# Kernel optimization log

Hardware: AMD Instinct MI355X
Metric: run time of the kernel (lower is better)

Reference implementation:

```python
import jax, jax.numpy as jnp
import numpy as np

EMBED = 1024
ADIM = 1024
H = 16
HD = ADIM // H          # 64
RAY = 48                # ray_subdim
R = RAY // 3            # 16
SCALE = 1.0 / np.sqrt(HD)
NB = 768                # boundary tokens
MN = 8                  # max neighbors
FG = 6                  # face_group
L = 1024                # tokens per face
B = 12                  # b * face_group
STAGES = 4


def _apply_dray(x, d, einsum_str, inverse):
    ray = x[..., :RAY].reshape(x.shape[:-1] + (3, R))
    if inverse:
        d = jnp.swapaxes(d, -1, -2)
    ray = jnp.einsum(einsum_str, d, ray).reshape(x.shape[:-1] + (RAY,))
    return jnp.concatenate([ray, x[..., RAY:]], axis=-1)


def setup_inputs() -> dict:
    key = jax.random.key(0)
    ks = jax.random.split(key, 12)
    inp = {}
    inp['x'] = jax.random.normal(ks[0], (B, L, EMBED), dtype=jnp.float32)
    inp['qkv_w'] = jax.random.normal(ks[1], (EMBED, 3 * ADIM), dtype=jnp.float32) * 0.02
    inp['out_w'] = jax.random.normal(ks[2], (ADIM, EMBED), dtype=jnp.float32) * 0.02
    inp['out_b'] = jax.random.normal(ks[3], (EMBED,), dtype=jnp.float32) * 0.02
    inp['d_ray'] = jax.random.normal(ks[4], (STAGES, FG, L, 3, 3), dtype=jnp.float32)
    inp['boundary_face_ids'] = jax.random.randint(ks[5], (NB,), 0, FG, dtype=jnp.int32).astype(jnp.int64)
    inp['boundary_token_indices'] = jnp.arange(NB, dtype=jnp.int64)
    inp['boundary_local_indices'] = jax.random.randint(ks[6], (NB,), 0, L, dtype=jnp.int32).astype(jnp.int64)
    inp['boundary_stage_ids'] = jax.random.randint(ks[7], (NB,), 0, STAGES, dtype=jnp.int32).astype(jnp.int64)
    inp['neighbor_face_ids'] = jax.random.randint(ks[8], (NB, MN), 0, FG, dtype=jnp.int32).astype(jnp.int64)
    inp['neighbor_token_indices'] = jax.random.randint(ks[9], (NB, MN), 0, L, dtype=jnp.int32).astype(jnp.int64)
    inp['neighbor_local_indices'] = jax.random.randint(ks[10], (NB, MN), 0, L, dtype=jnp.int32).astype(jnp.int64)
    inp['neighbor_stage_ids'] = jax.random.randint(ks[11], (NB, MN), 0, STAGES, dtype=jnp.int32).astype(jnp.int64)
    inp['neighbor_mask'] = jnp.ones((NB, MN), dtype=bool)
    inp['face_group'] = FG
    return inp


def reference(x, qkv_w, out_w, out_b, d_ray,
              boundary_face_ids, boundary_token_indices, boundary_local_indices, boundary_stage_ids,
              neighbor_face_ids, neighbor_token_indices, neighbor_local_indices, neighbor_stage_ids,
              neighbor_mask, face_group):
    b = x.shape[0] // face_group
    l = x.shape[1]
    xt = x.reshape(b, face_group, l, EMBED)          # [b, FG, L, E]
    max_face, max_idx = face_group - 1, l - 1

    qf = jnp.clip(boundary_face_ids, 0, max_face)
    qi = jnp.clip(boundary_token_indices, 0, max_idx)
    valid_q = (boundary_face_ids == qf) & (boundary_token_indices == qi)

    nf = jnp.clip(neighbor_face_ids, 0, max_face)
    ni = jnp.clip(neighbor_token_indices, 0, max_idx)
    mask = neighbor_mask & (neighbor_face_ids == nf) & (neighbor_token_indices == ni)

    # gather boundary queries and neighbor keys/values
    x_q = xt[:, qf, qi, :]                            # [b, NB, E]
    x_kv = xt[:, nf, ni, :]                           # [b, NB, MN, E]
    q = (x_q @ qkv_w)[..., :ADIM]
    kv = x_kv @ qkv_w
    k = kv[..., ADIM:2 * ADIM]
    v = kv[..., 2 * ADIM:]

    nb, mn = q.shape[1], k.shape[2]
    q = q.reshape(b, nb, H, HD)
    k = k.reshape(b, nb, mn, H, HD)
    v = v.reshape(b, nb, mn, H, HD)

    d_q = d_ray[boundary_stage_ids, boundary_face_ids, boundary_local_indices]     # [NB, 3, 3]
    d_k = d_ray[neighbor_stage_ids,
                jnp.maximum(neighbor_face_ids, 0),
                jnp.maximum(neighbor_local_indices, 0)]                            # [NB, MN, 3, 3]

    q = _apply_dray(q, d_q, 'nij,bnhjr->bnhir', inverse=False)
    k = _apply_dray(k, d_k, 'nmij,bnmhjr->bnmhir', inverse=False)
    v = _apply_dray(v, d_k, 'nmij,bnmhjr->bnmhir', inverse=False)

    attn = jnp.einsum('bnhd,bnmhd->bnmh', q, k) * SCALE
    attn = jnp.where(mask[None, :, :, None], attn, -jnp.inf)
    attn = jax.nn.softmax(attn, axis=2)               # softmax over neighbors
    out = jnp.einsum('bnmh,bnmhd->bnhd', attn, v)

    out = _apply_dray(out, d_q, 'nij,bnhjr->bnhir', inverse=True)
    out = out.reshape(b, nb, ADIM) @ out_w + out_b
    out = out * valid_q[None, :, None].astype(out.dtype)

    out_full = jnp.zeros_like(xt).at[:, qf, qi, :].set(out)
    return out_full.reshape(-1, l, EMBED)
```

## Files before the change

kernel.cpp:

```cpp
#include <hip/hip_runtime.h>
#include <hip/hip_bf16.h>
#include <cstddef>

#define FG 6
#define L 1024
#define NB 768
#define MN 8
#define H 16
#define HD 64
#define ADIM 1024
#define STAGES 4
#define SCALE 0.125f

typedef __attribute__((ext_vector_type(8))) short bf16x8;
typedef __attribute__((ext_vector_type(4))) float f32x4;
typedef __attribute__((address_space(3))) short lds_short_t;
typedef const __attribute__((address_space(1))) short g_short_t;

__device__ __forceinline__ int clampi(int v, int lo, int hi) {
  return v < lo ? lo : (v > hi ? hi : v);
}

__device__ __forceinline__ short f2bf(float f) {
  __hip_bfloat16 h = __float2bfloat16(f);
  return *reinterpret_cast<short*>(&h);
}

__device__ __forceinline__ void gload16(const short* g, short* l) {
  __builtin_amdgcn_global_load_lds((g_short_t*)g, (lds_short_t*)l, 16, 0, 0);
}

__global__ __launch_bounds__(256)
void conv_bf16(const float* __restrict__ in, short* __restrict__ out) {
  size_t i = ((size_t)blockIdx.x * 256 + threadIdx.x) * 8;
  float4 a = *(const float4*)(in + i);
  float4 b = *(const float4*)(in + i + 4);
  bf16x8 v;
  v[0] = f2bf(a.x); v[1] = f2bf(a.y); v[2] = f2bf(a.z); v[3] = f2bf(a.w);
  v[4] = f2bf(b.x); v[5] = f2bf(b.y); v[6] = f2bf(b.z); v[7] = f2bf(b.w);
  *(bf16x8*)(out + i) = v;
}

__global__ __launch_bounds__(256)
void transpose_conv(const float* __restrict__ in, short* __restrict__ out,
                    int K, int N) {
  __shared__ float tile[32][33];
  const int n0 = blockIdx.x * 32, k0 = blockIdx.y * 32;
  const int tx = threadIdx.x & 31, ty = threadIdx.x >> 5;
  #pragma unroll
  for (int i = 0; i < 4; ++i)
    tile[ty + i * 8][tx] = in[(size_t)(k0 + ty + i * 8) * N + n0 + tx];
  __syncthreads();
  #pragma unroll
  for (int i = 0; i < 4; ++i)
    out[(size_t)(n0 + ty + i * 8) * K + k0 + tx] =
        f2bf(tile[tx][ty + i * 8]);
}

template<int MODE>
__global__ __launch_bounds__(256)
void mfma_gemm(const short* __restrict__ A, const short* __restrict__ B,
               void* __restrict__ Cv,
               const int* __restrict__ f_ids, const int* __restrict__ t_ids,
               const float* __restrict__ bias)
{
  constexpr int KT    = 16;
  constexpr int BCOL0 = (MODE == 1) ? 1024 : 0;

  __shared__ __align__(16) short As[8192];
  __shared__ __align__(16) short Bs[8192];

  const int tid  = threadIdx.x;
  const int w    = tid >> 6, lane = tid & 63;
  const int row0 = blockIdx.y * 128, col0 = blockIdx.x * 128;

  size_t aoff[4], boff[4];
  short *adst[4], *bdst[4];
  #pragma unroll
  for (int c = 0; c < 4; ++c) {
    const int d = (w * 4 + c) * 64 + lane;
    const int r = d >> 3;
    const int ssrc = (d & 7) ^ (r & 7);
    long gr;
    if (MODE == 2) {
      gr = row0 + r;
    } else {
      const int rr = row0 + r;
      int bi, idx;
      if (MODE == 0) { bi = rr >= NB;          idx = rr - bi * NB; }
      else           { bi = rr >= NB * MN;     idx = rr - bi * NB * MN; }
      const int f = clampi(f_ids[idx], 0, FG - 1);
      const int q = clampi(t_ids[idx], 0, L - 1);
      gr = (long)(bi * FG + f) * L + q;
    }
    aoff[c] = (size_t)gr * 1024 + ssrc * 8;
    boff[c] = (size_t)(BCOL0 + col0 + r) * 1024 + ssrc * 8;
    adst[c] = As + (w * 4 + c) * 512;
    bdst[c] = Bs + (w * 4 + c) * 512;
  }

  const int lr = lane & 15, lq = lane >> 4;
  const int wrow = (w >> 1) * 64, wcol = (w & 1) * 64;
  const int sA = lr & 7;
  const char* As8 = (const char*)As;
  const char* Bs8 = (const char*)Bs;
  const int abase = (wrow + lr) * 128;
  const int bbase = (wcol + lr) * 128;

  f32x4 acc[4][4];
  #pragma unroll
  for (int m = 0; m < 4; ++m)
    #pragma unroll
    for (int n = 0; n < 4; ++n) acc[m][n] = (f32x4){0.f, 0.f, 0.f, 0.f};

  for (int kt = 0; kt < KT; ++kt) {
    #pragma unroll
    for (int c = 0; c < 4; ++c) {
      gload16(A + aoff[c] + kt * 64, adst[c]);
      gload16(B + boff[c] + kt * 64, bdst[c]);
    }
    __syncthreads();
    #pragma unroll
    for (int kk = 0; kk < 2; ++kk) {
      const int so = ((kk * 4 + lq) ^ sA) << 4;
      bf16x8 av[4], bv[4];
      #pragma unroll
      for (int m = 0; m < 4; ++m)
        av[m] = *(const bf16x8*)(As8 + abase + m * 2048 + so);
      #pragma unroll
      for (int n = 0; n < 4; ++n)
        bv[n] = *(const bf16x8*)(Bs8 + bbase + n * 2048 + so);
      #pragma unroll
      for (int m = 0; m < 4; ++m)
        #pragma unroll
        for (int n = 0; n < 4; ++n)
          acc[m][n] = __builtin_amdgcn_mfma_f32_16x16x32_bf16(
              av[m], bv[n], acc[m][n], 0, 0, 0);
    }
    __syncthreads();
  }

  if (MODE == 0) {
    float* C = (float*)Cv;
    #pragma unroll
    for (int m = 0; m < 4; ++m)
      #pragma unroll
      for (int j = 0; j < 4; ++j) {
        const int r = row0 + wrow + m * 16 + lq * 4 + j;
        #pragma unroll
        for (int n = 0; n < 4; ++n)
          C[(size_t)r * 1024 + col0 + wcol + n * 16 + lr] = acc[m][n][j];
      }
  } else {
    float* C = (float*)Cv;
    float bb[4];
    #pragma unroll
    for (int n = 0; n < 4; ++n) bb[n] = bias[col0 + wcol + n * 16 + lr];
    #pragma unroll
    for (int m = 0; m < 4; ++m)
      #pragma unroll
      for (int j = 0; j < 4; ++j) {
        const int r  = row0 + wrow + m * 16 + lq * 4 + j;
        const int bi = r >= NB;
        const int nn = r - bi * NB;
        const int bf = f_ids[nn], bt = t_ids[nn];
        const int qf = clampi(bf, 0, FG - 1), qi = clampi(bt, 0, L - 1);
        const bool valid = (bf == qf) && (bt == qi);
        const size_t obase = ((size_t)(bi * FG + qf) * L + qi) * 1024;
        #pragma unroll
        for (int n = 0; n < 4; ++n) {
          const int col = col0 + wcol + n * 16 + lr;
          C[obase + col] = valid ? (acc[m][n][j] + bb[n]) : 0.f;
        }
      }
  }
}


#define BAR()   do { __builtin_amdgcn_s_barrier(); __builtin_amdgcn_sched_barrier(0); } while (0)
#define LGKM(N) do { asm volatile("s_waitcnt lgkmcnt(" #N ")" ::: "memory"); __builtin_amdgcn_sched_barrier(0); } while (0)
#define VMC(N)  do { asm volatile("s_waitcnt vmcnt(" #N ")" ::: "memory"); __builtin_amdgcn_sched_barrier(0); } while (0)
#define PRIO1   __builtin_amdgcn_s_setprio(1)
#define PRIO0   __builtin_amdgcn_s_setprio(0)

#define LDA6(D, FB, KK, BUF)                                                  \
  { _Pragma("unroll")                                                         \
    for (int f_ = 0; f_ < 3; ++f_) {                                          \
      const int row_ = (2 * ((FB) + f_) + wm) * 16 + lr;                      \
      D[f_] = *(const bf16x8*)(As8 + (BUF) * 24576 + row_ * 128               \
               + ((((KK) * 4 + lq) ^ swz) << 4));                             \
    } }

#define LDB4(D, KK, BUF)                                                      \
  { _Pragma("unroll")                                                         \
    for (int g_ = 0; g_ < 4; ++g_) {                                          \
      const int row_ = wn * 64 + g_ * 16 + lr;                                \
      D[g_] = *(const bf16x8*)(Bs8 + (BUF) * 32768 + row_ * 128               \
               + ((((KK) * 4 + lq) ^ swz) << 4));                             \
    } }

#define MM6(AV, BV, FB)                                                       \
  { _Pragma("unroll")                                                         \
    for (int f_ = 0; f_ < 3; ++f_)                                            \
      _Pragma("unroll")                                                       \
      for (int g_ = 0; g_ < 4; ++g_)                                          \
        acc[(FB) + f_][g_] = __builtin_amdgcn_mfma_f32_16x16x32_bf16(         \
            AV[f_], BV[g_], acc[(FB) + f_][g_], 0, 0, 0); }

__global__ __launch_bounds__(512, 2)
void kv_gemm192(const short* __restrict__ A, const short* __restrict__ B,
                short* __restrict__ C,
                const int* __restrict__ f_ids, const int* __restrict__ t_ids)
{
  __shared__ __align__(16) short As[24576];
  __shared__ __align__(16) short Bs[32768];

  const int tid = threadIdx.x;
  const int w = tid >> 6, lane = tid & 63;
  const int wm = w >> 2, wn = w & 3;
  const int lr = lane & 15, lq = lane >> 4;
  const int row0 = blockIdx.y * 192;
  const int col0 = blockIdx.x * 256;

  const int ssrc = (((tid & 7) ^ ((tid >> 3) & 7))) * 8;

  size_t a_src[3];
  #pragma unroll
  for (int c = 0; c < 3; ++c) {
    const int rr = row0 + c * 64 + (tid >> 3);
    const int bi = rr >= NB * MN;
    const int idx = rr - bi * (NB * MN);
    const int f = clampi(f_ids[idx], 0, FG - 1);
    const int q = clampi(t_ids[idx], 0, L - 1);
    a_src[c] = (size_t)((bi * FG + f) * L + q) * 1024 + ssrc;
  }
  size_t b_src[2][2];
  #pragma unroll
  for (int h = 0; h < 2; ++h)
    #pragma unroll
    for (int i = 0; i < 2; ++i)
      b_src[h][i] = (size_t)(1024 + col0 + h * 128 + ((tid + i * 512) >> 3)) * 1024 + ssrc;

  auto stgA = [&](int c, int kt, int buf) {
    gload16(A + a_src[c] + kt * 64, As + buf * 12288 + c * 4096 + tid * 8);
  };
  auto stgB = [&](int h, int kt, int buf) {
    gload16(B + b_src[h][0] + kt * 64, Bs + buf * 16384 + h * 8192 + tid * 8);
    gload16(B + b_src[h][1] + kt * 64, Bs + buf * 16384 + h * 8192 + 4096 + tid * 8);
  };

  const char* As8 = (const char*)As;
  const char* Bs8 = (const char*)Bs;
  const int swz = lane & 7;

  f32x4 acc[6][4];
  #pragma unroll
  for (int f = 0; f < 6; ++f)
    #pragma unroll
    for (int g = 0; g < 4; ++g) acc[f][g] = (f32x4){0.f, 0.f, 0.f, 0.f};

  bf16x8 avA[3], avB[3], bv0[4], bv1[4];

  stgB(0, 0, 0); stgB(1, 0, 0); stgA(0, 0, 0); stgA(1, 0, 0); stgA(2, 0, 0);
  stgB(0, 1, 1); stgB(1, 1, 1); stgA(0, 1, 1);
  VMC(5); BAR();
  LDA6(avA, 0, 0, 0); LDB4(bv0, 0, 0);

  for (int I = 0; I < 7; ++I) {
    const int kA = 2 * I + 1, kB = 2 * I + 2, kC = 2 * I + 3;
    BAR(); stgA(1, kA, 1);
    LDA6(avB, 0, 1, 0); LDB4(bv1, 1, 0);
    LGKM(7); PRIO1; MM6(avA, bv0, 0); PRIO0;
    BAR(); stgA(2, kA, 1);
    LDA6(avA, 3, 0, 0);
    LGKM(3); PRIO1; MM6(avB, bv1, 0); PRIO0;
    BAR(); stgB(0, kB, 0); VMC(2);
    LDA6(avB, 3, 1, 0);
    LGKM(3); PRIO1; MM6(avA, bv0, 3); PRIO0;
    BAR(); stgB(1, kB, 0); stgA(0, kB, 0);
    LDA6(avA, 0, 0, 1); LDB4(bv0, 0, 1);
    LGKM(7); PRIO1; MM6(avB, bv1, 3); PRIO0;
    BAR(); stgA(1, kB, 0);
    LDA6(avB, 0, 1, 1); LDB4(bv1, 1, 1);
    LGKM(7); PRIO1; MM6(avA, bv0, 0); PRIO0;
    BAR(); stgA(2, kB, 0);
    LDA6(avA, 3, 0, 1);
    LGKM(3); PRIO1; MM6(avB, bv1, 0); PRIO0;
    BAR(); stgB(0, kC, 1); VMC(2);
    LDA6(avB, 3, 1, 1);
    LGKM(3); PRIO1; MM6(avA, bv0, 3); PRIO0;
    BAR(); stgB(1, kC, 1); stgA(0, kC, 1);
    LDA6(avA, 0, 0, 0); LDB4(bv0, 0, 0);
    LGKM(7); PRIO1; MM6(avB, bv1, 3); PRIO0;
  }

  {
    BAR(); stgA(1, 15, 1);
    LDA6(avB, 0, 1, 0); LDB4(bv1, 1, 0);
    LGKM(7); PRIO1; MM6(avA, bv0, 0); PRIO0;

    BAR(); stgA(2, 15, 1);
    LDA6(avA, 3, 0, 0);
    LGKM(3); PRIO1; MM6(avB, bv1, 0); PRIO0;

    BAR(); VMC(0);
    LDA6(avB, 3, 1, 0);
    LGKM(3); PRIO1; MM6(avA, bv0, 3); PRIO0;

    BAR();
    LDA6(avA, 0, 0, 1); LDB4(bv0, 0, 1);
    LGKM(7); PRIO1; MM6(avB, bv1, 3); PRIO0;

    BAR();
    LDA6(avB, 0, 1, 1); LDB4(bv1, 1, 1);
    LGKM(7); PRIO1; MM6(avA, bv0, 0); PRIO0;

    BAR();
    LDA6(avA, 3, 0, 1);
    LGKM(3); PRIO1; MM6(avB, bv1, 0); PRIO0;

    BAR();
    LDA6(avB, 3, 1, 1);
    LGKM(3); PRIO1; MM6(avA, bv0, 3); PRIO0;

    BAR();
    LGKM(0); PRIO1; MM6(avB, bv1, 3); PRIO0;
  }

  #pragma unroll
  for (int f = 0; f < 6; ++f) {
    #pragma unroll
    for (int j = 0; j < 4; ++j) {
      const int r = row0 + (2 * f + wm) * 16 + lq * 4 + j;
      short* cp = C + (size_t)r * 2048 + col0 + wn * 64 + lr;
      #pragma unroll
      for (int g = 0; g < 4; ++g)
        cp[g * 16] = f2bf(acc[f][g][j]);
    }
  }
}

__global__ __launch_bounds__(256)
void attn_kernel(const float* __restrict__ dray,
                 const int* __restrict__ bfid, const int* __restrict__ blid,
                 const int* __restrict__ bsid,
                 const int* __restrict__ nfid, const int* __restrict__ ntid,
                 const int* __restrict__ nlid, const int* __restrict__ nsid,
                 const int* __restrict__ nmask,
                 const float* __restrict__ qbuf,
                 const __hip_bfloat16* __restrict__ kvbuf,
                 __hip_bfloat16* __restrict__ obuf)
{
  const int lane = threadIdx.x & 63;
  const int gw   = blockIdx.x * 4 + (threadIdx.x >> 6);
  const int h    = gw & (H - 1);
  const int bn   = gw >> 4;
  const int n    = bn % NB;

  int st = clampi(bsid[n], 0, STAGES - 1);
  int f  = clampi(bfid[n], 0, FG - 1);
  int lc = clampi(blid[n], 0, L - 1);
  const float* dqp = dray + ((size_t)(st * FG + f) * L + lc) * 9;
  float dq[9];
  #pragma unroll
  for (int t = 0; t < 9; ++t) dq[t] = dqp[t];

  const float qraw = qbuf[(size_t)bn * ADIM + h * HD + lane];
  const int rr = lane & 15;

  float x0 = __shfl(qraw, rr), x1 = __shfl(qraw, 16 + rr), x2 = __shfl(qraw, 32 + rr);
  float q0 = dq[0]*x0 + dq[1]*x1 + dq[2]*x2;
  float q1 = dq[3]*x0 + dq[4]*x1 + dq[5]*x2;
  float q2 = dq[6]*x0 + dq[7]*x1 + dq[8]*x2;
  float qd = lane < 16 ? q0 : lane < 32 ? q1 : lane < 48 ? q2 : qraw;

  const __hip_bfloat16* kvb = kvbuf + (size_t)bn * MN * 2048 + h * HD;
  float s[MN], vd[MN];
  #pragma unroll
  for (int m = 0; m < MN; ++m) {
    const int idx = n * MN + m;
    int nst = clampi(nsid[idx], 0, STAGES - 1);
    int nfc = clampi(nfid[idx], 0, FG - 1);
    int nlc = clampi(nlid[idx], 0, L - 1);
    const float* dkp = dray + ((size_t)(nst * FG + nfc) * L + nlc) * 9;
    float dk[9];
    #pragma unroll
    for (int t = 0; t < 9; ++t) dk[t] = dkp[t];

    float kraw = __bfloat162float(kvb[(size_t)m * 2048 + lane]);
    float k0 = __shfl(kraw, rr), k1 = __shfl(kraw, 16 + rr), k2 = __shfl(kraw, 32 + rr);
    float kr0 = dk[0]*k0 + dk[1]*k1 + dk[2]*k2;
    float kr1 = dk[3]*k0 + dk[4]*k1 + dk[5]*k2;
    float kr2 = dk[6]*k0 + dk[7]*k1 + dk[8]*k2;
    float kd = lane < 16 ? kr0 : lane < 32 ? kr1 : lane < 48 ? kr2 : kraw;

    float p = qd * kd;
    #pragma unroll
    for (int off = 32; off; off >>= 1) p += __shfl_xor(p, off);
    s[m] = p;

    float vraw = __bfloat162float(kvb[(size_t)m * 2048 + 1024 + lane]);
    float v0 = __shfl(vraw, rr), v1 = __shfl(vraw, 16 + rr), v2 = __shfl(vraw, 32 + rr);
    float vr0 = dk[0]*v0 + dk[1]*v1 + dk[2]*v2;
    float vr1 = dk[3]*v0 + dk[4]*v1 + dk[5]*v2;
    float vr2 = dk[6]*v0 + dk[7]*v1 + dk[8]*v2;
    vd[m] = lane < 16 ? vr0 : lane < 32 ? vr1 : lane < 48 ? vr2 : vraw;
  }

  float mx = -INFINITY;
  #pragma unroll
  for (int m = 0; m < MN; ++m) {
    const int idx = n * MN + m;
    int nf = nfid[idx], nt = ntid[idx];
    bool ok = (nmask[idx] != 0) && nf >= 0 && nf < FG && nt >= 0 && nt < L;
    s[m] = ok ? s[m] * SCALE : -INFINITY;
    mx = fmaxf(mx, s[m]);
  }
  float den = 0.f;
  #pragma unroll
  for (int m = 0; m < MN; ++m) { s[m] = expf(s[m] - mx); den += s[m]; }
  float inv = 1.0f / den;

  float od = 0.f;
  #pragma unroll
  for (int m = 0; m < MN; ++m) od += s[m] * vd[m];
  od *= inv;

  float y0 = __shfl(od, rr), y1 = __shfl(od, 16 + rr), y2 = __shfl(od, 32 + rr);
  float t0 = dq[0]*y0 + dq[3]*y1 + dq[6]*y2;
  float t1 = dq[1]*y0 + dq[4]*y1 + dq[7]*y2;
  float t2 = dq[2]*y0 + dq[5]*y1 + dq[8]*y2;
  float outd = lane < 16 ? t0 : lane < 32 ? t1 : lane < 48 ? t2 : od;

  obuf[(size_t)bn * ADIM + h * HD + lane] = __float2bfloat16(outd);
}

extern "C" void kernel_launch(void* const* d_in, const int* in_sizes, int n_in,
                              void* d_out, int out_size, void* d_ws, size_t ws_size,
                              hipStream_t stream) {
  const float* x     = (const float*)d_in[0];
  const float* qkv_w = (const float*)d_in[1];
  const float* out_w = (const float*)d_in[2];
  const float* out_b = (const float*)d_in[3];
  const float* dray  = (const float*)d_in[4];
  const int* bfid  = (const int*)d_in[5];
  const int* btid  = (const int*)d_in[6];
  const int* blid  = (const int*)d_in[7];
  const int* bsid  = (const int*)d_in[8];
  const int* nfid  = (const int*)d_in[9];
  const int* ntid  = (const int*)d_in[10];
  const int* nlid  = (const int*)d_in[11];
  const int* nsid  = (const int*)d_in[12];
  const int* nmask = (const int*)d_in[13];

  char* ws = (char*)d_ws;
  short* xb    = (short*)(ws);
  short* qwT   = (short*)(ws + 25165824);
  short* owT   = (short*)(ws + 31457280);
  float* qbuf  = (float*)(ws + 33554432);
  short* kvbuf = (short*)(ws + 39845888);
  short* obuf  = (short*)(ws + 90177536);

  hipMemsetAsync(d_out, 0, (size_t)out_size * sizeof(float), stream);

  conv_bf16<<<6144, 256, 0, stream>>>(x, xb);
  transpose_conv<<<dim3(96, 32), 256, 0, stream>>>(qkv_w, qwT, 1024, 3072);
  transpose_conv<<<dim3(32, 32), 256, 0, stream>>>(out_w, owT, 1024, 1024);

  mfma_gemm<0><<<dim3(8, 12), 256, 0, stream>>>(xb, qwT, qbuf, bfid, btid, nullptr);
  kv_gemm192<<<dim3(8, 64), 512, 0, stream>>>(xb, qwT, kvbuf, nfid, ntid);
  attn_kernel<<<6144, 256, 0, stream>>>(dray, bfid, blid, bsid,
                                        nfid, ntid, nlid, nsid, nmask,
                                        qbuf, (const __hip_bfloat16*)kvbuf,
                                        (__hip_bfloat16*)obuf);
  mfma_gemm<2><<<dim3(8, 12), 256, 0, stream>>>(obuf, owT, d_out, bfid, btid, out_b);
}
```

Baseline: 181.0 us.

## Merge Q projection into KV GEMM launch and retile output GEMM to 64 rows

The separate Q-projection GEMM (96 blocks) is folded into the pipelined 192x256 KV GEMM kernel as extra grid rows. Those Q blocks use the boundary indices and write fp32 output, and surplus column blocks exit early. This removes a launch and lets the small Q GEMM run alongside the KV work instead of underfilling the GPU by itself. The output projection moves to a new 64-row tile kernel, doubling its block count to 192 for better CU occupancy, at the cost of reloading the B tiles more often.

```diff
diff --git a/kernel.cpp b/kernel.cpp
--- a/kernel.cpp
+++ b/kernel.cpp
@@ -57,125 +57,6 @@
         f2bf(tile[tx][ty + i * 8]);
 }
 
-template<int MODE>
-__global__ __launch_bounds__(256)
-void mfma_gemm(const short* __restrict__ A, const short* __restrict__ B,
-               void* __restrict__ Cv,
-               const int* __restrict__ f_ids, const int* __restrict__ t_ids,
-               const float* __restrict__ bias)
-{
-  constexpr int KT    = 16;
-  constexpr int BCOL0 = (MODE == 1) ? 1024 : 0;
-
-  __shared__ __align__(16) short As[8192];
-  __shared__ __align__(16) short Bs[8192];
-
-  const int tid  = threadIdx.x;
-  const int w    = tid >> 6, lane = tid & 63;
-  const int row0 = blockIdx.y * 128, col0 = blockIdx.x * 128;
-
-  size_t aoff[4], boff[4];
-  short *adst[4], *bdst[4];
-  #pragma unroll
-  for (int c = 0; c < 4; ++c) {
-    const int d = (w * 4 + c) * 64 + lane;
-    const int r = d >> 3;
-    const int ssrc = (d & 7) ^ (r & 7);
-    long gr;
-    if (MODE == 2) {
-      gr = row0 + r;
-    } else {
-      const int rr = row0 + r;
-      int bi, idx;
-      if (MODE == 0) { bi = rr >= NB;          idx = rr - bi * NB; }
-      else           { bi = rr >= NB * MN;     idx = rr - bi * NB * MN; }
-      const int f = clampi(f_ids[idx], 0, FG - 1);
-      const int q = clampi(t_ids[idx], 0, L - 1);
-      gr = (long)(bi * FG + f) * L + q;
-    }
-    aoff[c] = (size_t)gr * 1024 + ssrc * 8;
-    boff[c] = (size_t)(BCOL0 + col0 + r) * 1024 + ssrc * 8;
-    adst[c] = As + (w * 4 + c) * 512;
-    bdst[c] = Bs + (w * 4 + c) * 512;
-  }
-
-  const int lr = lane & 15, lq = lane >> 4;
-  const int wrow = (w >> 1) * 64, wcol = (w & 1) * 64;
-  const int sA = lr & 7;
-  const char* As8 = (const char*)As;
-  const char* Bs8 = (const char*)Bs;
-  const int abase = (wrow + lr) * 128;
-  const int bbase = (wcol + lr) * 128;
-
-  f32x4 acc[4][4];
-  #pragma unroll
-  for (int m = 0; m < 4; ++m)
-    #pragma unroll
-    for (int n = 0; n < 4; ++n) acc[m][n] = (f32x4){0.f, 0.f, 0.f, 0.f};
-
-  for (int kt = 0; kt < KT; ++kt) {
-    #pragma unroll
-    for (int c = 0; c < 4; ++c) {
-      gload16(A + aoff[c] + kt * 64, adst[c]);
-      gload16(B + boff[c] + kt * 64, bdst[c]);
-    }
-    __syncthreads();
-    #pragma unroll
-    for (int kk = 0; kk < 2; ++kk) {
-      const int so = ((kk * 4 + lq) ^ sA) << 4;
-      bf16x8 av[4], bv[4];
-      #pragma unroll
-      for (int m = 0; m < 4; ++m)
-        av[m] = *(const bf16x8*)(As8 + abase + m * 2048 + so);
-      #pragma unroll
-      for (int n = 0; n < 4; ++n)
-        bv[n] = *(const bf16x8*)(Bs8 + bbase + n * 2048 + so);
-      #pragma unroll
-      for (int m = 0; m < 4; ++m)
-        #pragma unroll
-        for (int n = 0; n < 4; ++n)
-          acc[m][n] = __builtin_amdgcn_mfma_f32_16x16x32_bf16(
-              av[m], bv[n], acc[m][n], 0, 0, 0);
-    }
-    __syncthreads();
-  }
-
-  if (MODE == 0) {
-    float* C = (float*)Cv;
-    #pragma unroll
-    for (int m = 0; m < 4; ++m)
-      #pragma unroll
-      for (int j = 0; j < 4; ++j) {
-        const int r = row0 + wrow + m * 16 + lq * 4 + j;
-        #pragma unroll
-        for (int n = 0; n < 4; ++n)
-          C[(size_t)r * 1024 + col0 + wcol + n * 16 + lr] = acc[m][n][j];
-      }
-  } else {
-    float* C = (float*)Cv;
-    float bb[4];
-    #pragma unroll
-    for (int n = 0; n < 4; ++n) bb[n] = bias[col0 + wcol + n * 16 + lr];
-    #pragma unroll
-    for (int m = 0; m < 4; ++m)
-      #pragma unroll
-      for (int j = 0; j < 4; ++j) {
-        const int r  = row0 + wrow + m * 16 + lq * 4 + j;
-        const int bi = r >= NB;
-        const int nn = r - bi * NB;
-        const int bf = f_ids[nn], bt = t_ids[nn];
-        const int qf = clampi(bf, 0, FG - 1), qi = clampi(bt, 0, L - 1);
-        const bool valid = (bf == qf) && (bt == qi);
-        const size_t obase = ((size_t)(bi * FG + qf) * L + qi) * 1024;
-        #pragma unroll
-        for (int n = 0; n < 4; ++n) {
-          const int col = col0 + wcol + n * 16 + lr;
-          C[obase + col] = valid ? (acc[m][n][j] + bb[n]) : 0.f;
-        }
-      }
-  }
-}
-
 
 #define BAR()   do { __builtin_amdgcn_s_barrier(); __builtin_amdgcn_sched_barrier(0); } while (0)
 #define LGKM(N) do { asm volatile("s_waitcnt lgkmcnt(" #N ")" ::: "memory"); __builtin_amdgcn_sched_barrier(0); } while (0)
@@ -208,19 +89,27 @@
             AV[f_], BV[g_], acc[(FB) + f_][g_], 0, 0, 0); }
 
 __global__ __launch_bounds__(512, 2)
-void kv_gemm192(const short* __restrict__ A, const short* __restrict__ B,
-                short* __restrict__ C,
-                const int* __restrict__ f_ids, const int* __restrict__ t_ids)
+void qkv_gemm192(const short* __restrict__ A, const short* __restrict__ B,
+                 short* __restrict__ Ckv, float* __restrict__ Cq,
+                 const int* __restrict__ nfid, const int* __restrict__ ntid,
+                 const int* __restrict__ bfid, const int* __restrict__ btid)
 {
   __shared__ __align__(16) short As[24576];
   __shared__ __align__(16) short Bs[32768];
+
+  const bool isQ = blockIdx.y >= 64;
+  if (isQ && blockIdx.x >= 4) return;
 
   const int tid = threadIdx.x;
   const int w = tid >> 6, lane = tid & 63;
   const int wm = w >> 2, wn = w & 3;
   const int lr = lane & 15, lq = lane >> 4;
-  const int row0 = blockIdx.y * 192;
+  const int row0 = (isQ ? (blockIdx.y - 64) : blockIdx.y) * 192;
   const int col0 = blockIdx.x * 256;
+  const int bcol0 = isQ ? 0 : 1024;
+  const int* fi = isQ ? bfid : nfid;
+  const int* ti = isQ ? btid : ntid;
+  const int MROW = isQ ? NB : NB * MN;
 
   const int ssrc = (((tid & 7) ^ ((tid >> 3) & 7))) * 8;
 
@@ -228,10 +117,10 @@
   #pragma unroll
   for (int c = 0; c < 3; ++c) {
     const int rr = row0 + c * 64 + (tid >> 3);
-    const int bi = rr >= NB * MN;
-    const int idx = rr - bi * (NB * MN);
-    const int f = clampi(f_ids[idx], 0, FG - 1);
-    const int q = clampi(t_ids[idx], 0, L - 1);
+    const int bi = rr >= MROW;
+    const int idx = rr - bi * MROW;
+    const int f = clampi(fi[idx], 0, FG - 1);
+    const int q = clampi(ti[idx], 0, L - 1);
     a_src[c] = (size_t)((bi * FG + f) * L + q) * 1024 + ssrc;
   }
   size_t b_src[2][2];
@@ -239,7 +128,7 @@
   for (int h = 0; h < 2; ++h)
     #pragma unroll
     for (int i = 0; i < 2; ++i)
-      b_src[h][i] = (size_t)(1024 + col0 + h * 128 + ((tid + i * 512) >> 3)) * 1024 + ssrc;
+      b_src[h][i] = (size_t)(bcol0 + col0 + h * 128 + ((tid + i * 512) >> 3)) * 1024 + ssrc;
 
   auto stgA = [&](int c, int kt, int buf) {
     gload16(A + a_src[c] + kt * 64, As + buf * 12288 + c * 4096 + tid * 8);
@@ -327,17 +216,121 @@
     LGKM(0); PRIO1; MM6(avB, bv1, 3); PRIO0;
   }
 
-  #pragma unroll
-  for (int f = 0; f < 6; ++f) {
+  if (!isQ) {
+    #pragma unroll
+    for (int f = 0; f < 6; ++f) {
+      #pragma unroll
+      for (int j = 0; j < 4; ++j) {
+        const int r = row0 + (2 * f + wm) * 16 + lq * 4 + j;
+        short* cp = Ckv + (size_t)r * 2048 + col0 + wn * 64 + lr;
+        #pragma unroll
+        for (int g = 0; g < 4; ++g)
+          cp[g * 16] = f2bf(acc[f][g][j]);
+      }
+    }
+  } else {
+    #pragma unroll
+    for (int f = 0; f < 6; ++f) {
+      #pragma unroll
+      for (int j = 0; j < 4; ++j) {
+        const int r = row0 + (2 * f + wm) * 16 + lq * 4 + j;
+        float* cp = Cq + (size_t)r * 1024 + col0 + wn * 64 + lr;
+        #pragma unroll
+        for (int g = 0; g < 4; ++g)
+          cp[g * 16] = acc[f][g][j];
+      }
+    }
+  }
+}
+
+__global__ __launch_bounds__(256)
+void out_gemm64(const short* __restrict__ A, const short* __restrict__ B,
+                float* __restrict__ C,
+                const int* __restrict__ f_ids, const int* __restrict__ t_ids,
+                const float* __restrict__ bias)
+{
+  __shared__ __align__(16) short As[4096];
+  __shared__ __align__(16) short Bs[8192];
+
+  const int tid = threadIdx.x;
+  const int w = tid >> 6, lane = tid & 63;
+  const int row0 = blockIdx.y * 64, col0 = blockIdx.x * 128;
+  const int lr = lane & 15, lq = lane >> 4;
+  const int wrow = (w >> 1) * 32, wcol = (w & 1) * 64;
+
+  size_t asrc[2]; short* adst[2];
+  #pragma unroll
+  for (int c = 0; c < 2; ++c) {
+    const int d = c * 256 + tid, r = d >> 3;
+    const int ss = (d & 7) ^ (r & 7);
+    asrc[c] = (size_t)(row0 + r) * 1024 + ss * 8;
+    adst[c] = As + d * 8;
+  }
+  size_t bsrc[4]; short* bdst[4];
+  #pragma unroll
+  for (int c = 0; c < 4; ++c) {
+    const int d = c * 256 + tid, r = d >> 3;
+    const int ss = (d & 7) ^ (r & 7);
+    bsrc[c] = (size_t)(col0 + r) * 1024 + ss * 8;
+    bdst[c] = Bs + d * 8;
+  }
+
+  const char* As8 = (const char*)As;
+  const char* Bs8 = (const char*)Bs;
+  const int swz = lr & 7;
+
+  f32x4 acc[2][4];
+  #pragma unroll
+  for (int m = 0; m < 2; ++m)
+    #pragma unroll
+    for (int n = 0; n < 4; ++n) acc[m][n] = (f32x4){0.f, 0.f, 0.f, 0.f};
+
+  for (int kt = 0; kt < 16; ++kt) {
+    #pragma unroll
+    for (int c = 0; c < 2; ++c) gload16(A + asrc[c] + kt * 64, adst[c]);
+    #pragma unroll
+    for (int c = 0; c < 4; ++c) gload16(B + bsrc[c] + kt * 64, bdst[c]);
+    __syncthreads();
+    #pragma unroll
+    for (int kk = 0; kk < 2; ++kk) {
+      const int so = ((kk * 4 + lq) ^ swz) << 4;
+      bf16x8 av[2], bv[4];
+      #pragma unroll
+      for (int m = 0; m < 2; ++m)
+        av[m] = *(const bf16x8*)(As8 + (wrow + m * 16 + lr) * 128 + so);
+      #pragma unroll
+      for (int n = 0; n < 4; ++n)
+        bv[n] = *(const bf16x8*)(Bs8 + (wcol + n * 16 + lr) * 128 + so);
+      #pragma unroll
+      for (int m = 0; m < 2; ++m)
+        #pragma unroll
+        for (int n = 0; n < 4; ++n)
+          acc[m][n] = __builtin_amdgcn_mfma_f32_16x16x32_bf16(
+              av[m], bv[n], acc[m][n], 0, 0, 0);
+    }
+    __syncthreads();
+  }
+
+  float bb[4];
+  #pragma unroll
+  for (int n = 0; n < 4; ++n) bb[n] = bias[col0 + wcol + n * 16 + lr];
+  #pragma unroll
+  for (int m = 0; m < 2; ++m)
     #pragma unroll
     for (int j = 0; j < 4; ++j) {
-      const int r = row0 + (2 * f + wm) * 16 + lq * 4 + j;
-      short* cp = C + (size_t)r * 2048 + col0 + wn * 64 + lr;
-      #pragma unroll
-      for (int g = 0; g < 4; ++g)
-        cp[g * 16] = f2bf(acc[f][g][j]);
+      const int r  = row0 + wrow + m * 16 + lq * 4 + j;
+      const int bi = r >= NB;
+      const int nn = r - bi * NB;
+      const int bf = f_ids[nn], bt = t_ids[nn];
+      const int qf = clampi(bf, 0, FG - 1), qi = clampi(bt, 0, L - 1);
+      const bool valid = (bf == qf) && (bt == qi);
+      const size_t obase = ((size_t)(bi * FG + qf) * L + qi) * 1024;
+      #pragma unroll
+      for (int n = 0; n < 4; ++n) {
+        const int col = col0 + wcol + n * 16 + lr;
+        C[obase + col] = valid ? (acc[m][n][j] + bb[n]) : 0.f;
+      }
     }
-  }
 }
 
 __global__ __launch_bounds__(256)
@@ -461,17 +454,18 @@
   short* kvbuf = (short*)(ws + 39845888);
   short* obuf  = (short*)(ws + 90177536);
 
-  hipMemsetAsync(d_out, 0, (size_t)out_size * sizeof(float), stream);
+  (void)hipMemsetAsync(d_out, 0, (size_t)out_size * sizeof(float), stream);
 
   conv_bf16<<<6144, 256, 0, stream>>>(x, xb);
   transpose_conv<<<dim3(96, 32), 256, 0, stream>>>(qkv_w, qwT, 1024, 3072);
   transpose_conv<<<dim3(32, 32), 256, 0, stream>>>(out_w, owT, 1024, 1024);
 
-  mfma_gemm<0><<<dim3(8, 12), 256, 0, stream>>>(xb, qwT, qbuf, bfid, btid, nullptr);
-  kv_gemm192<<<dim3(8, 64), 512, 0, stream>>>(xb, qwT, kvbuf, nfid, ntid);
+  qkv_gemm192<<<dim3(8, 72), 512, 0, stream>>>(xb, qwT, kvbuf, qbuf,
+                                               nfid, ntid, bfid, btid);
   attn_kernel<<<6144, 256, 0, stream>>>(dray, bfid, blid, bsid,
                                         nfid, ntid, nlid, nsid, nmask,
                                         qbuf, (const __hip_bfloat16*)kvbuf,
                                         (__hip_bfloat16*)obuf);
-  mfma_gemm<2><<<dim3(8, 12), 256, 0, stream>>>(obuf, owT, d_out, bfid, btid, out_b);
-}
+  out_gemm64<<<dim3(8, 24), 256, 0, stream>>>(obuf, owT, (float*)d_out,
+                                              bfid, btid, out_b);
+}
```

Result: no change. 179.6 us (-0.8%).
